# Kernel tuning notes

Measured on AMD Instinct MI355X. Metric: run time of the kernel, lower is better.

The kernel has to match this reference:

```python
import jax, jax.numpy as jnp
import numpy as np

NAN_VALUE = -1.0
ALPHA = 0.5
EPS = 1e-6
MAX_HEIGHT = 30
NBINS = MAX_HEIGHT + 1  # 1m bins [0,1)...[29,30) plus [30, inf)
SHAPE = (64, 512, 512)


def setup_inputs() -> dict:
    key = jax.random.key(0)
    k1, k2, k3 = jax.random.split(key, 3)
    # natural-space heights in [0, 40) m, transformed to log1p space
    heights = jax.random.uniform(k1, SHAPE, minval=0.0, maxval=40.0)
    target = jnp.log1p(heights)
    invalid = jax.random.uniform(k2, SHAPE) < 0.1
    target = jnp.where(invalid, NAN_VALUE, target).astype(jnp.float32)
    pred = (target + 0.1 * jax.random.normal(k3, SHAPE)).astype(jnp.float32)
    return {"pred": pred, "target": target}


def reference(pred, target):
    valid = target != NAN_VALUE                       # [B,H,W] bool
    nat = jnp.expm1(target)                           # natural-space heights
    in_range = valid & (nat >= 0.0)                   # pixels that fall in some height range
    bins = jnp.clip(jnp.floor(nat), 0.0, MAX_HEIGHT).astype(jnp.int32)  # bin 30 == [30, inf)

    total_valid = jnp.sum(valid.astype(jnp.float32))
    # histogram of valid pixels over the 31 height ranges (single scatter-add)
    counts = jax.ops.segment_sum(
        jnp.where(in_range, 1.0, 0.0).ravel(), bins.ravel(), num_segments=NBINS
    )
    freq = jax.lax.stop_gradient(counts / total_valid)      # frequencies are data, not grads
    w = 1.0 / (freq ** ALPHA + EPS)                          # inverse-frequency weights, [31]

    pix_w = jnp.where(in_range, w[bins], 0.0)                # per-pixel weight; 0 outside ranges/invalid
    base = jnp.abs(pred - target)
    # mean over valid pixels of weighted L1 (pixels in no range contribute 0, as in torch)
    return jnp.sum(base * pix_w) / total_valid
```

## Files before the change

kernel.cpp:

```cpp
#include <hip/hip_runtime.h>
#include <math.h>


#define NBLK   2048
#define NTHR   256
#define NROW   128
#define HS     33
#define FSCALE 32768.0f
#define CSHIFT 24

__global__ __launch_bounds__(256) void fused_kernel(const float* __restrict__ pred,
                                                    const float* __restrict__ target,
                                                    unsigned long long* __restrict__ g_part,
                                                    int n4, int nblk) {
    __shared__ unsigned int lh[NROW * HS];
    const int tid = threadIdx.x;
    for (int k = tid; k < NROW * HS; k += NTHR) lh[k] = 0u;
    __syncthreads();

    const float4* t4 = (const float4*)target;
    const float4* p4 = (const float4*)pred;
    const int row = (tid & (NROW - 1)) * HS;
    const int S = nblk * NTHR;

    for (int i = blockIdx.x * NTHR + tid; i < n4; i += S) {
        float4 tv = t4[i];
        float4 pv = p4[i];
#pragma unroll
        for (int e = 0; e < 4; ++e) {
            float t = (&tv.x)[e];
            float p = (&pv.x)[e];
            if (t >= 0.0f) {
                float ex = __builtin_amdgcn_exp2f(t * 1.4426950408889634f);
                int b = min((int)ex, 31) - 1;
                unsigned int fx = (unsigned int)(fabsf(p - t) * FSCALE + 0.5f);
                atomicAdd(&lh[row + b], fx | (1u << CSHIFT));
            }
        }
    }

    __syncthreads();
    if (tid < 31) {
        unsigned int cnt = 0, sum = 0;
#pragma unroll 8
        for (int r = 0; r < NROW; ++r) {
            unsigned int v = lh[r * HS + tid];
            cnt += v >> CSHIFT;
            sum += v & 0x00FFFFFFu;
        }
        g_part[blockIdx.x * 32 + tid] = ((unsigned long long)cnt << 40) | (unsigned long long)sum;
    } else if (tid == 31) {
        g_part[blockIdx.x * 32 + 31] = 0ull;
    }
}

__global__ __launch_bounds__(1024) void reduce_kernel(const unsigned long long* __restrict__ g_part,
                                                      float* __restrict__ out, int nblk) {
    __shared__ unsigned long long ssum[32][32];
    __shared__ unsigned int      scnt[32][32];
    const int tid = threadIdx.x;
    const int col = tid & 31, grp = tid >> 5;

    unsigned long long sum = 0;
    unsigned int cnt = 0;
    for (int r = grp; r < nblk; r += 32) {
        unsigned long long v = g_part[r * 32 + col];
        sum += v & ((1ull << 40) - 1ull);
        cnt += (unsigned int)(v >> 40);
    }
    ssum[grp][col] = sum;
    scnt[grp][col] = cnt;
    __syncthreads();

    if (tid < 64) {
        unsigned long long s = 0;
        unsigned int c = 0;
        if (tid < 31) {
#pragma unroll
            for (int g = 0; g < 32; ++g) { s += ssum[g][tid]; c += scnt[g][tid]; }
        }
        unsigned int ctot = c;
#pragma unroll
        for (int off = 32; off > 0; off >>= 1) ctot += __shfl_xor(ctot, off, 64);
        float tv = (float)ctot;
        double term = 0.0;
        if (tid < 31) {
            float freq = (float)c / tv;
            float w    = 1.0f / (sqrtf(freq) + 1e-6f);
            term = (double)s * (double)w;
        }
#pragma unroll
        for (int off = 32; off > 0; off >>= 1) term += __shfl_down(term, off, 64);
        if (tid == 0) out[0] = (float)(term / 32768.0 / (double)tv);
    }
}

extern "C" void kernel_launch(void* const* d_in, const int* in_sizes, int n_in,
                              void* d_out, int out_size, void* d_ws, size_t ws_size,
                              hipStream_t stream) {
    const float* pred   = (const float*)d_in[0];
    const float* target = (const float*)d_in[1];
    float*       out    = (float*)d_out;

    unsigned long long* g_part = (unsigned long long*)d_ws;

    const int n  = in_sizes[0];
    const int n4 = n / 4;

    int nblk = NBLK;
    size_t need = (size_t)nblk * 32 * sizeof(unsigned long long);
    if (ws_size < need) nblk = (int)(ws_size / (32 * sizeof(unsigned long long)));

    fused_kernel<<<nblk, NTHR, 0, stream>>>(pred, target, g_part, n4, nblk);
    reduce_kernel<<<1, 1024, 0, stream>>>(g_part, out, nblk);
}
```

Baseline: 48.26 us.

## Replace LDS atomic histogram with packed per-thread register histograms

Each thread now keeps 31 bins in 16 registers, two bins per word, each bin holding a 6-bit count and a 10-bit fixed-point sum. Bins are updated with predicated adds instead of shared-memory atomics, and the grid-stride loop is unrolled two-way. The histogram is then reduced through LDS in two stages. This removes atomic contention in LDS, but the fixed-point scale drops from 32768 to 32, which coarsens precision. The narrow fields also rely on each thread seeing few elements with small errors, so other sizes or distributions could overflow and corrupt neighbouring fields.

```diff
diff --git a/kernel.cpp b/kernel.cpp
--- a/kernel.cpp
+++ b/kernel.cpp
@@ -2,52 +2,78 @@
 #include <math.h>
 
 
-#define NBLK   2048
-#define NTHR   256
-#define NROW   128
-#define HS     33
-#define FSCALE 32768.0f
-#define CSHIFT 24
+#define NBLK  2048
+#define NTHR  256
+#define SCALE 32.0
+
+__device__ __forceinline__ void process4(const float4& tv, const float4& pv,
+                                         unsigned int* acc) {
+#pragma unroll
+    for (int e = 0; e < 4; ++e) {
+        float t = (&tv.x)[e];
+        float p = (&pv.x)[e];
+        float ex = __builtin_amdgcn_exp2f(t * 1.4426950408889634f);
+        int b  = min((int)ex, 31) - 1;
+        int b1 = b >> 1;
+        unsigned int val = (unsigned int)fmaf(fabsf(p - t), 32.0f, 0.5f);
+        unsigned int inc = (1024u | val) << ((b & 1) << 4);
+#pragma unroll
+        for (int r = 0; r < 16; ++r)
+            acc[r] += (b1 == r) ? inc : 0u;
+    }
+}
 
 __global__ __launch_bounds__(256) void fused_kernel(const float* __restrict__ pred,
                                                     const float* __restrict__ target,
                                                     unsigned long long* __restrict__ g_part,
                                                     int n4, int nblk) {
-    __shared__ unsigned int lh[NROW * HS];
+    __shared__ unsigned int lhe[NTHR * 17];
+    __shared__ unsigned int pc[8][32], ps[8][32];
     const int tid = threadIdx.x;
-    for (int k = tid; k < NROW * HS; k += NTHR) lh[k] = 0u;
-    __syncthreads();
+
+    unsigned int acc[16];
+#pragma unroll
+    for (int r = 0; r < 16; ++r) acc[r] = 0u;
 
     const float4* t4 = (const float4*)target;
     const float4* p4 = (const float4*)pred;
-    const int row = (tid & (NROW - 1)) * HS;
     const int S = nblk * NTHR;
 
-    for (int i = blockIdx.x * NTHR + tid; i < n4; i += S) {
-        float4 tv = t4[i];
-        float4 pv = p4[i];
+    int i = blockIdx.x * NTHR + tid;
+    for (; i + S < n4; i += 2 * S) {
+        float4 tv0 = t4[i],     pv0 = p4[i];
+        float4 tv1 = t4[i + S], pv1 = p4[i + S];
+        process4(tv0, pv0, acc);
+        process4(tv1, pv1, acc);
+    }
+    for (; i < n4; i += S) {
+        float4 tv = t4[i], pv = p4[i];
+        process4(tv, pv, acc);
+    }
+
 #pragma unroll
-        for (int e = 0; e < 4; ++e) {
-            float t = (&tv.x)[e];
-            float p = (&pv.x)[e];
-            if (t >= 0.0f) {
-                float ex = __builtin_amdgcn_exp2f(t * 1.4426950408889634f);
-                int b = min((int)ex, 31) - 1;
-                unsigned int fx = (unsigned int)(fabsf(p - t) * FSCALE + 0.5f);
-                atomicAdd(&lh[row + b], fx | (1u << CSHIFT));
+    for (int r = 0; r < 16; ++r) lhe[tid * 17 + r] = acc[r];
+    __syncthreads();
+
+    {
+        const int g = tid >> 5, l = tid & 31;
+        unsigned int cnt = 0, sum = 0;
+        if (l < 31) {
+            const int w = l >> 1, sh = (l & 1) << 4;
+            for (int row = g * 32; row < g * 32 + 32; ++row) {
+                unsigned int v = (lhe[row * 17 + w] >> sh) & 0xFFFFu;
+                cnt += v >> 10;
+                sum += v & 0x3FFu;
             }
         }
+        pc[g][l] = cnt;
+        ps[g][l] = sum;
     }
-
     __syncthreads();
     if (tid < 31) {
         unsigned int cnt = 0, sum = 0;
-#pragma unroll 8
-        for (int r = 0; r < NROW; ++r) {
-            unsigned int v = lh[r * HS + tid];
-            cnt += v >> CSHIFT;
-            sum += v & 0x00FFFFFFu;
-        }
+#pragma unroll
+        for (int g = 0; g < 8; ++g) { cnt += pc[g][tid]; sum += ps[g][tid]; }
         g_part[blockIdx.x * 32 + tid] = ((unsigned long long)cnt << 40) | (unsigned long long)sum;
     } else if (tid == 31) {
         g_part[blockIdx.x * 32 + 31] = 0ull;
@@ -91,7 +117,7 @@
         }
 #pragma unroll
         for (int off = 32; off > 0; off >>= 1) term += __shfl_down(term, off, 64);
-        if (tid == 0) out[0] = (float)(term / 32768.0 / (double)tv);
+        if (tid == 0) out[0] = (float)(term / SCALE / (double)tv);
     }
 }
 
```

Measured after the change: 55.67 us. 15.3% more time.

## Replace shared-memory atomic histogram with per-thread cumulative threshold counters

Applied to the files above, without the earlier changes.

Each element is now compared against 31 precomputed log1p bin thresholds with inline asm, so per-thread registers hold cumulative counts and L1 sums. The reduce kernel recovers per-bin values by differencing adjacent cumulative totals. This removes the exp2 and the LDS atomic per element, and it switches the sums from fixed-point to float. The cost is about 124 VALU instructions per element, heavy register pressure, and a block count halved to 1024.

```diff
diff --git a/kernel.cpp b/kernel.cpp
--- a/kernel.cpp
+++ b/kernel.cpp
@@ -2,96 +2,177 @@
 #include <math.h>
 
 
-#define NBLK   2048
-#define NTHR   256
-#define NROW   128
-#define HS     33
-#define FSCALE 32768.0f
-#define CSHIFT 24
+#define NBLK 1024
+#define NTHR 256
+
+#define ACC4(c0,c1,c2,c3, s0,s1,s2,s3, t, d, h0,h1,h2,h3)                      \
+  { float tmp_;                                                                \
+    asm("v_cmp_le_f32 vcc, %11, %9\n\t"                                        \
+        "v_cndmask_b32 %8, 0, %10, vcc\n\t"                                    \
+        "v_add_f32 %4, %4, %8\n\t"                                             \
+        "v_addc_co_u32 %0, vcc, 0, %0, vcc\n\t"                                \
+        "v_cmp_le_f32 vcc, %12, %9\n\t"                                        \
+        "v_cndmask_b32 %8, 0, %10, vcc\n\t"                                    \
+        "v_add_f32 %5, %5, %8\n\t"                                             \
+        "v_addc_co_u32 %1, vcc, 0, %1, vcc\n\t"                                \
+        "v_cmp_le_f32 vcc, %13, %9\n\t"                                        \
+        "v_cndmask_b32 %8, 0, %10, vcc\n\t"                                    \
+        "v_add_f32 %6, %6, %8\n\t"                                             \
+        "v_addc_co_u32 %2, vcc, 0, %2, vcc\n\t"                                \
+        "v_cmp_le_f32 vcc, %14, %9\n\t"                                        \
+        "v_cndmask_b32 %8, 0, %10, vcc\n\t"                                    \
+        "v_add_f32 %7, %7, %8\n\t"                                             \
+        "v_addc_co_u32 %3, vcc, 0, %3, vcc"                                    \
+        : "+v"(c0), "+v"(c1), "+v"(c2), "+v"(c3),                              \
+          "+v"(s0), "+v"(s1), "+v"(s2), "+v"(s3), "=&v"(tmp_)                  \
+        : "v"(t), "v"(d), "s"(h0), "s"(h1), "s"(h2), "s"(h3)                   \
+        : "vcc"); }
+
+#define ACC3(c0,c1,c2, s0,s1,s2, t, d, h0,h1,h2)                               \
+  { float tmp_;                                                                \
+    asm("v_cmp_le_f32 vcc, %9, %7\n\t"                                         \
+        "v_cndmask_b32 %6, 0, %8, vcc\n\t"                                     \
+        "v_add_f32 %3, %3, %6\n\t"                                             \
+        "v_addc_co_u32 %0, vcc, 0, %0, vcc\n\t"                                \
+        "v_cmp_le_f32 vcc, %10, %7\n\t"                                        \
+        "v_cndmask_b32 %6, 0, %8, vcc\n\t"                                     \
+        "v_add_f32 %4, %4, %6\n\t"                                             \
+        "v_addc_co_u32 %1, vcc, 0, %1, vcc\n\t"                                \
+        "v_cmp_le_f32 vcc, %11, %7\n\t"                                        \
+        "v_cndmask_b32 %6, 0, %8, vcc\n\t"                                     \
+        "v_add_f32 %5, %5, %6\n\t"                                             \
+        "v_addc_co_u32 %2, vcc, 0, %2, vcc"                                    \
+        : "+v"(c0), "+v"(c1), "+v"(c2),                                        \
+          "+v"(s0), "+v"(s1), "+v"(s2), "=&v"(tmp_)                            \
+        : "v"(t), "v"(d), "s"(h0), "s"(h1), "s"(h2)                            \
+        : "vcc"); }
 
 __global__ __launch_bounds__(256) void fused_kernel(const float* __restrict__ pred,
                                                     const float* __restrict__ target,
-                                                    unsigned long long* __restrict__ g_part,
+                                                    unsigned int* __restrict__ g_cnt,
+                                                    float* __restrict__ g_sum,
                                                     int n4, int nblk) {
-    __shared__ unsigned int lh[NROW * HS];
+    const float T0=0.0f,         T1=0.69314718f,  T2=1.09861229f,  T3=1.38629436f,
+                T4=1.60943791f,  T5=1.79175947f,  T6=1.94591015f,  T7=2.07944154f,
+                T8=2.19722458f,  T9=2.30258509f,  T10=2.39789527f, T11=2.48490665f,
+                T12=2.56494936f, T13=2.63905733f, T14=2.70805020f, T15=2.77258872f,
+                T16=2.83321334f, T17=2.89037176f, T18=2.94443898f, T19=2.99573227f,
+                T20=3.04452244f, T21=3.09104245f, T22=3.13549422f, T23=3.17805383f,
+                T24=3.21887582f, T25=3.25809654f, T26=3.29583687f, T27=3.33220451f,
+                T28=3.36729583f, T29=3.40119738f, T30=3.43398720f;
+
+    __shared__ unsigned int lhs[NTHR * 33];
+    __shared__ unsigned int pa[8][32];
+    __shared__ float        pb[8][32];
     const int tid = threadIdx.x;
-    for (int k = tid; k < NROW * HS; k += NTHR) lh[k] = 0u;
-    __syncthreads();
+
+    unsigned int c[31];
+    float        s[31];
+#pragma unroll
+    for (int k = 0; k < 31; ++k) { c[k] = 0u; s[k] = 0.0f; }
 
     const float4* t4 = (const float4*)target;
     const float4* p4 = (const float4*)pred;
-    const int row = (tid & (NROW - 1)) * HS;
-    const int S = nblk * NTHR;
 
-    for (int i = blockIdx.x * NTHR + tid; i < n4; i += S) {
+    for (int i = blockIdx.x * NTHR + tid; i < n4; i += nblk * NTHR) {
         float4 tv = t4[i];
         float4 pv = p4[i];
 #pragma unroll
         for (int e = 0; e < 4; ++e) {
             float t = (&tv.x)[e];
-            float p = (&pv.x)[e];
-            if (t >= 0.0f) {
-                float ex = __builtin_amdgcn_exp2f(t * 1.4426950408889634f);
-                int b = min((int)ex, 31) - 1;
-                unsigned int fx = (unsigned int)(fabsf(p - t) * FSCALE + 0.5f);
-                atomicAdd(&lh[row + b], fx | (1u << CSHIFT));
-            }
+            float d = fabsf((&pv.x)[e] - t);
+            ACC4(c[0],c[1],c[2],c[3],     s[0],s[1],s[2],s[3],     t, d, T0,T1,T2,T3)
+            ACC4(c[4],c[5],c[6],c[7],     s[4],s[5],s[6],s[7],     t, d, T4,T5,T6,T7)
+            ACC4(c[8],c[9],c[10],c[11],   s[8],s[9],s[10],s[11],   t, d, T8,T9,T10,T11)
+            ACC4(c[12],c[13],c[14],c[15], s[12],s[13],s[14],s[15], t, d, T12,T13,T14,T15)
+            ACC4(c[16],c[17],c[18],c[19], s[16],s[17],s[18],s[19], t, d, T16,T17,T18,T19)
+            ACC4(c[20],c[21],c[22],c[23], s[20],s[21],s[22],s[23], t, d, T20,T21,T22,T23)
+            ACC4(c[24],c[25],c[26],c[27], s[24],s[25],s[26],s[27], t, d, T24,T25,T26,T27)
+            ACC3(c[28],c[29],c[30],       s[28],s[29],s[30],       t, d, T28,T29,T30)
         }
     }
 
+#pragma unroll
+    for (int k = 0; k < 31; ++k) lhs[tid * 33 + k] = c[k];
+    __syncthreads();
+    {   const int g = tid >> 5, l = tid & 31;
+        unsigned int a = 0;
+        if (l < 31) {
+#pragma unroll 8
+            for (int r = g * 32; r < g * 32 + 32; ++r) a += lhs[r * 33 + l];
+        }
+        pa[g][l] = a;
+    }
     __syncthreads();
     if (tid < 31) {
-        unsigned int cnt = 0, sum = 0;
+        unsigned int a = 0;
+#pragma unroll
+        for (int g = 0; g < 8; ++g) a += pa[g][tid];
+        g_cnt[blockIdx.x * 32 + tid] = a;
+    } else if (tid == 31) {
+        g_cnt[blockIdx.x * 32 + 31] = 0u;
+    }
+    __syncthreads();
+#pragma unroll
+    for (int k = 0; k < 31; ++k) ((float*)lhs)[tid * 33 + k] = s[k];
+    __syncthreads();
+    {   const int g = tid >> 5, l = tid & 31;
+        float a = 0.0f;
+        if (l < 31) {
 #pragma unroll 8
-        for (int r = 0; r < NROW; ++r) {
-            unsigned int v = lh[r * HS + tid];
-            cnt += v >> CSHIFT;
-            sum += v & 0x00FFFFFFu;
+            for (int r = g * 32; r < g * 32 + 32; ++r) a += ((float*)lhs)[r * 33 + l];
         }
-        g_part[blockIdx.x * 32 + tid] = ((unsigned long long)cnt << 40) | (unsigned long long)sum;
+        pb[g][l] = a;
+    }
+    __syncthreads();
+    if (tid < 31) {
+        float a = 0.0f;
+#pragma unroll
+        for (int g = 0; g < 8; ++g) a += pb[g][tid];
+        g_sum[blockIdx.x * 32 + tid] = a;
     } else if (tid == 31) {
-        g_part[blockIdx.x * 32 + 31] = 0ull;
+        g_sum[blockIdx.x * 32 + 31] = 0.0f;
     }
 }
 
-__global__ __launch_bounds__(1024) void reduce_kernel(const unsigned long long* __restrict__ g_part,
+__global__ __launch_bounds__(1024) void reduce_kernel(const unsigned int* __restrict__ g_cnt,
+                                                      const float* __restrict__ g_sum,
                                                       float* __restrict__ out, int nblk) {
-    __shared__ unsigned long long ssum[32][32];
-    __shared__ unsigned int      scnt[32][32];
-    const int tid = threadIdx.x;
-    const int col = tid & 31, grp = tid >> 5;
+    __shared__ unsigned int sc[32][33];
+    __shared__ double       sd[32][33];
+    __shared__ unsigned int totc[32];
+    __shared__ double       tots[32];
+    const int tid = threadIdx.x, col = tid & 31, grp = tid >> 5;
 
-    unsigned long long sum = 0;
-    unsigned int cnt = 0;
+    unsigned int cacc = 0;
+    double       sacc = 0.0;
     for (int r = grp; r < nblk; r += 32) {
-        unsigned long long v = g_part[r * 32 + col];
-        sum += v & ((1ull << 40) - 1ull);
-        cnt += (unsigned int)(v >> 40);
+        cacc += g_cnt[r * 32 + col];
+        sacc += (double)g_sum[r * 32 + col];
     }
-    ssum[grp][col] = sum;
-    scnt[grp][col] = cnt;
+    sc[grp][col] = cacc;
+    sd[grp][col] = sacc;
     __syncthreads();
-
+    if (tid < 32) {
+        unsigned int cC = 0; double sS = 0.0;
+#pragma unroll
+        for (int g = 0; g < 32; ++g) { cC += sc[g][tid]; sS += sd[g][tid]; }
+        totc[tid] = cC; tots[tid] = sS;
+    }
+    __syncthreads();
     if (tid < 64) {
-        unsigned long long s = 0;
-        unsigned int c = 0;
+        double term = 0.0;
+        float tv = (float)totc[0];
         if (tid < 31) {
-#pragma unroll
-            for (int g = 0; g < 32; ++g) { s += ssum[g][tid]; c += scnt[g][tid]; }
-        }
-        unsigned int ctot = c;
-#pragma unroll
-        for (int off = 32; off > 0; off >>= 1) ctot += __shfl_xor(ctot, off, 64);
-        float tv = (float)ctot;
-        double term = 0.0;
-        if (tid < 31) {
-            float freq = (float)c / tv;
+            unsigned int cb = totc[tid] - ((tid < 30) ? totc[tid + 1] : 0u);
+            double       sb = tots[tid] - ((tid < 30) ? tots[tid + 1] : 0.0);
+            float freq = (float)cb / tv;
             float w    = 1.0f / (sqrtf(freq) + 1e-6f);
-            term = (double)s * (double)w;
+            term = sb * (double)w;
         }
 #pragma unroll
         for (int off = 32; off > 0; off >>= 1) term += __shfl_down(term, off, 64);
-        if (tid == 0) out[0] = (float)(term / 32768.0 / (double)tv);
+        if (tid == 0) out[0] = (float)(term / (double)tv);
     }
 }
 
@@ -102,15 +183,16 @@
     const float* target = (const float*)d_in[1];
     float*       out    = (float*)d_out;
 
-    unsigned long long* g_part = (unsigned long long*)d_ws;
-
     const int n  = in_sizes[0];
     const int n4 = n / 4;
 
     int nblk = NBLK;
-    size_t need = (size_t)nblk * 32 * sizeof(unsigned long long);
-    if (ws_size < need) nblk = (int)(ws_size / (32 * sizeof(unsigned long long)));
+    size_t need = (size_t)nblk * 32 * 4 * 2;
+    if (ws_size < need) nblk = (int)(ws_size / (32 * 4 * 2));
 
-    fused_kernel<<<nblk, NTHR, 0, stream>>>(pred, target, g_part, n4, nblk);
-    reduce_kernel<<<1, 1024, 0, stream>>>(g_part, out, nblk);
+    unsigned int* g_cnt = (unsigned int*)d_ws;
+    float*        g_sum = (float*)((char*)d_ws + (size_t)nblk * 32 * 4);
+
+    fused_kernel<<<nblk, NTHR, 0, stream>>>(pred, target, g_cnt, g_sum, n4, nblk);
+    reduce_kernel<<<1, 1024, 0, stream>>>(g_cnt, g_sum, out, nblk);
 }
```

Measured after the change: 67.96 us. +40.8%, slower.
